# Performance work log

Measured on AMD Instinct MI355X. Metric: run time of the kernel, lower is better.

## Reference

```python
import jax, jax.numpy as jnp
import numpy as np

D_MODEL = 512
NUM_HEADS = 8
D_HEAD = 64
BATCH = 2
SEQ = 2048
NEG_BIG = 1.0e10


def setup_inputs() -> dict:
    key = jax.random.key(0)
    k1, k2, k3, k4, k5 = jax.random.split(key, 5)
    scale = D_MODEL ** -0.5
    return {
        "x": jax.random.normal(k1, (BATCH, SEQ, D_MODEL), dtype=jnp.float32),
        "W_Q": jax.random.normal(k2, (NUM_HEADS, D_HEAD, D_MODEL), dtype=jnp.float32) * scale,
        "W_K": jax.random.normal(k3, (NUM_HEADS, D_HEAD, D_MODEL), dtype=jnp.float32) * scale,
        "W_V": jax.random.normal(k4, (NUM_HEADS, D_HEAD, D_MODEL), dtype=jnp.float32) * scale,
        "W_O": jax.random.normal(k5, (D_MODEL, D_HEAD * NUM_HEADS), dtype=jnp.float32) * scale,
    }


def reference(x, W_Q, W_K, W_V, W_O):
    b, n, d = x.shape
    # q,k,v: [b, heads, pos, d_head]
    q = jnp.einsum('ihd,bpd->biph', W_Q, x)
    k = jnp.einsum('ihd,bpd->biph', W_K, x)
    v = jnp.einsum('ihd,bpd->biph', W_V, x)
    # scores: [b, heads, q_pos, k_pos]
    scores = jnp.einsum('biph,biqh->biqp', k, q)
    tril = jnp.tril(jnp.ones((n, n), dtype=scores.dtype))   # keep p <= q
    triu = jnp.triu(jnp.ones((n, n), dtype=scores.dtype))   # buffer 'mask'
    # Faithful to source: tril(scores) - 1e10 * (1 - triu)
    masked = scores * tril - NEG_BIG * (1.0 - triu)
    attn = jax.nn.softmax(masked / (D_HEAD ** 0.5), axis=-1)
    z = jnp.einsum('biph,biqp->biqh', v, attn)               # [b, i, q, h]
    z_flat = jnp.transpose(z, (0, 2, 1, 3)).reshape(b, n, -1)  # [b, q, i*h]
    out = jnp.einsum('df,bqf->bqd', W_O, z_flat)
    return out
```

## Files before the change

kernel.cpp:

```cpp
#include <hip/hip_runtime.h>
#include <stdint.h>

#define BATCH 2
#define SEQ 2048
#define DM 512
#define NH 8
#define DH 64
#define MROWS (BATCH * SEQ)
#define NCHUNK 64
#define CHUNK (SEQ / NCHUNK)

typedef __attribute__((ext_vector_type(8))) short bf16x8;
typedef __attribute__((ext_vector_type(4))) float f32x4;

__device__ __forceinline__ unsigned short f2bf(float f) {
    union { float f; uint32_t u; } x; x.f = f;
    uint32_t r = x.u + 0x7fffu + ((x.u >> 16) & 1u);
    return (unsigned short)(r >> 16);
}
__device__ __forceinline__ float bf2f(unsigned short s) {
    union { uint32_t u; float f; } x; x.u = ((uint32_t)s) << 16;
    return x.f;
}

__device__ __forceinline__ void gl_lds16(const void* g, void* l) {
    __builtin_amdgcn_global_load_lds(
        (const __attribute__((address_space(1))) void*)(uintptr_t)g,
        (__attribute__((address_space(3))) void*)(uint32_t)(uintptr_t)l,
        16, 0, 0);
}

__global__ void cvt_all(const float4* __restrict__ x,
                        const float4* __restrict__ Wq, const float4* __restrict__ Wk,
                        const float4* __restrict__ Wv, const float4* __restrict__ Wo,
                        ushort4* __restrict__ xb, ushort4* __restrict__ wb) {
    int i = blockIdx.x * blockDim.x + threadIdx.x;
    float4 v; ushort4* dst; int off;
    if (i < 524288) {
        v = x[i]; dst = xb; off = i;
    } else {
        int j = i - 524288;
        if (j < 131072) {
            int head = j >> 14, rp = (j >> 7) & 127, colq = j & 127;
            v = (rp < 64) ? Wq[head * 8192 + rp * 128 + colq]
                          : Wk[head * 8192 + (rp - 64) * 128 + colq];
        } else if (j < 196608) {
            v = Wv[j - 131072];
        } else {
            v = Wo[j - 196608];
        }
        dst = wb; off = j;
    }
    ushort4 o; o.x = f2bf(v.x); o.y = f2bf(v.y); o.z = f2bf(v.z); o.w = f2bf(v.w);
    dst[off] = o;
}

__global__ __launch_bounds__(256) void proj(
    const unsigned short* __restrict__ xb, const unsigned short* __restrict__ wb,
    float* __restrict__ cA, float* __restrict__ cW,
    unsigned short* __restrict__ V, float* __restrict__ csum)
{
    __shared__ __align__(16) unsigned short S[256 * 32];
    const int t = threadIdx.x, lane = t & 63, wave = t >> 6;
    const int lr = lane >> 2, lc = (lane & 3) * 8;
    const int bid = blockIdx.x;
    const int wm = wave * 32;
    const int kcol = (lane >> 4) * 8;
    const int l15 = lane & 15;

    if (bid < 256) {
        const int head = bid & 7, m0 = (bid >> 3) * 128;
        const unsigned short* B = wb + head * 65536;
        const unsigned short* gb[4];
#pragma unroll
        for (int r = 0; r < 4; r++) {
            int grow = r * 64 + wave * 16 + lr;
            gb[r] = (grow < 128) ? xb + (size_t)(m0 + grow) * 512 + lc
                                 : B + (size_t)(grow - 128) * 512 + lc;
        }
        f32x4 acc[2][8];
#pragma unroll
        for (int i = 0; i < 2; i++)
#pragma unroll
            for (int j = 0; j < 8; j++) { f32x4 z = {0.f,0.f,0.f,0.f}; acc[i][j] = z; }
        for (int k0 = 0; k0 < 512; k0 += 32) {
            __syncthreads();
#pragma unroll
            for (int r = 0; r < 4; r++)
                gl_lds16(gb[r] + k0, S + (r * 64 + wave * 16) * 32);
            __syncthreads();
            bf16x8 af[2], bfr[8];
#pragma unroll
            for (int i = 0; i < 2; i++)
                af[i] = *(const bf16x8*)(S + (wm + i * 16 + l15) * 32 + kcol);
#pragma unroll
            for (int j = 0; j < 8; j++)
                bfr[j] = *(const bf16x8*)(S + (128 + j * 16 + l15) * 32 + kcol);
#pragma unroll
            for (int i = 0; i < 2; i++)
#pragma unroll
                for (int j = 0; j < 8; j++)
                    acc[i][j] = __builtin_amdgcn_mfma_f32_16x16x32_bf16(af[i], bfr[j], acc[i][j], 0, 0, 0);
        }
#pragma unroll
        for (int i = 0; i < 2; i++)
#pragma unroll
            for (int r = 0; r < 4; r++) {
                float d = 0.f;
#pragma unroll
                for (int j = 0; j < 4; j++) d += acc[i][j][r] * acc[i][j + 4][r];
                d += __shfl_xor(d, 1); d += __shfl_xor(d, 2);
                d += __shfl_xor(d, 4); d += __shfl_xor(d, 8);
                if (l15 == 0) {
                    int row = m0 + wm + i * 16 + (lane >> 4) * 4 + r;
                    int p = row & (SEQ - 1);
                    float dd = d * 0.125f;
                    float M = fmaxf(dd, 0.f);
                    float a = expf(dd - M), e0 = expf(-M);
                    float Z = a + (float)(SEQ - 1 - p) * e0;
                    cA[row * NH + head] = a / Z;
                    cW[row * NH + head] = e0 / Z;
                }
            }
    } else {
        const int b2 = bid - 256;
        const int head = b2 & 7, m0 = (b2 >> 3) * 128, n0 = head * 64;
        const unsigned short* B = wb + 524288 + (size_t)n0 * 512;
        const unsigned short* gb[3];
#pragma unroll
        for (int r = 0; r < 3; r++) {
            int grow = r * 64 + wave * 16 + lr;
            gb[r] = (grow < 128) ? xb + (size_t)(m0 + grow) * 512 + lc
                                 : B + (size_t)(grow - 128) * 512 + lc;
        }
        f32x4 acc[2][4];
#pragma unroll
        for (int i = 0; i < 2; i++)
#pragma unroll
            for (int j = 0; j < 4; j++) { f32x4 z = {0.f,0.f,0.f,0.f}; acc[i][j] = z; }
        for (int k0 = 0; k0 < 512; k0 += 32) {
            __syncthreads();
#pragma unroll
            for (int r = 0; r < 3; r++)
                gl_lds16(gb[r] + k0, S + (r * 64 + wave * 16) * 32);
            __syncthreads();
            bf16x8 af[2], bfr[4];
#pragma unroll
            for (int i = 0; i < 2; i++)
                af[i] = *(const bf16x8*)(S + (wm + i * 16 + l15) * 32 + kcol);
#pragma unroll
            for (int j = 0; j < 4; j++)
                bfr[j] = *(const bf16x8*)(S + (128 + j * 16 + l15) * 32 + kcol);
#pragma unroll
            for (int i = 0; i < 2; i++)
#pragma unroll
                for (int j = 0; j < 4; j++)
                    acc[i][j] = __builtin_amdgcn_mfma_f32_16x16x32_bf16(af[i], bfr[j], acc[i][j], 0, 0, 0);
        }
        const int crow = m0 + wm + (lane >> 4) * 4;
#pragma unroll
        for (int i = 0; i < 2; i++)
#pragma unroll
            for (int j = 0; j < 4; j++)
#pragma unroll
                for (int r = 0; r < 4; r++)
                    V[(size_t)(crow + i * 16 + r) * DM + n0 + j * 16 + l15] = f2bf(acc[i][j][r]);
        float s[4];
#pragma unroll
        for (int j = 0; j < 4; j++) {
            s[j] = 0.f;
#pragma unroll
            for (int i = 0; i < 2; i++)
#pragma unroll
                for (int r = 0; r < 4; r++) s[j] += acc[i][j][r];
            s[j] += __shfl_xor(s[j], 16);
            s[j] += __shfl_xor(s[j], 32);
        }
        if (lane < 16) {
            int bi = (m0 >> 11) * NH + head;
            int chunk = ((m0 & (SEQ - 1)) >> 5) + wave;
#pragma unroll
            for (int j = 0; j < 4; j++)
                csum[(bi * NCHUNK + chunk) * 64 + j * 16 + lane] = s[j];
        }
    }
}

__global__ __launch_bounds__(256) void zbuild(
    const unsigned short* __restrict__ V, const float* __restrict__ csum,
    const float* __restrict__ cA, const float* __restrict__ cW,
    unsigned short* __restrict__ Zb) {
    int ci = blockIdx.x * 4 + (threadIdx.x >> 6);
    int h = threadIdx.x & 63;
    int c = ci & (NCHUNK - 1), bi = ci >> 6;
    int i = bi & 7, b = bi >> 3;
    float r = 0.f;
    for (int cc = c + 1; cc < NCHUNK; cc++) r += csum[((bi << 6) + cc) * 64 + h];
    for (int j = CHUNK - 1; j >= 0; j--) {
        int p = c * CHUNK + j;
        size_t row = (size_t)(b * SEQ + p);
        float v = bf2f(V[row * DM + i * DH + h]);
        float a = cA[row * NH + i], w = cW[row * NH + i];
        Zb[row * DM + i * DH + h] = f2bf(fmaf(a, v, w * r));
        r += v;
    }
}

template<int TM, int TN, int WM, int WN>
__global__ __launch_bounds__(256) void gemm_bt(
    const unsigned short* __restrict__ A, const unsigned short* __restrict__ B,
    float* __restrict__ C, int M, int N, int K)
{
    constexpr int ROWS = TM + TN;
    constexpr int ROUNDS = ROWS / 64;
    constexpr int MI = WM / 16, NJ = WN / 16;
    constexpr int WAVES_N = TN / WN;
    __shared__ __align__(16) unsigned short S[ROWS * 32];
    const int t = threadIdx.x, lane = t & 63, wave = t >> 6;
    const int wm = (wave / WAVES_N) * WM, wn = (wave % WAVES_N) * WN;
    const int m0 = blockIdx.x * TM, n0 = blockIdx.y * TN;
    const int lr = lane >> 2, lc = (lane & 3) * 8;

    const unsigned short* gbase[ROUNDS];
#pragma unroll
    for (int r = 0; r < ROUNDS; r++) {
        int grow = r * 64 + wave * 16 + lr;
        gbase[r] = (grow < TM) ? A + (size_t)(m0 + grow) * K + lc
                               : B + (size_t)(n0 + grow - TM) * K + lc;
    }

    f32x4 acc[MI][NJ];
#pragma unroll
    for (int i = 0; i < MI; i++)
#pragma unroll
        for (int j = 0; j < NJ; j++) { f32x4 z = {0.f,0.f,0.f,0.f}; acc[i][j] = z; }

    const int mrow = wm + (lane & 15);
    const int nrow = TM + wn + (lane & 15);
    const int kcol = (lane >> 4) * 8;

    for (int k0 = 0; k0 < K; k0 += 32) {
        __syncthreads();
#pragma unroll
        for (int r = 0; r < ROUNDS; r++)
            gl_lds16(gbase[r] + k0, S + (r * 64 + wave * 16) * 32);
        __syncthreads();
        bf16x8 af[MI], bfr[NJ];
#pragma unroll
        for (int i = 0; i < MI; i++)
            af[i] = *(const bf16x8*)(S + (mrow + i * 16) * 32 + kcol);
#pragma unroll
        for (int j = 0; j < NJ; j++)
            bfr[j] = *(const bf16x8*)(S + (nrow + j * 16) * 32 + kcol);
#pragma unroll
        for (int i = 0; i < MI; i++)
#pragma unroll
            for (int j = 0; j < NJ; j++)
                acc[i][j] = __builtin_amdgcn_mfma_f32_16x16x32_bf16(af[i], bfr[j], acc[i][j], 0, 0, 0);
    }
    const int crow = m0 + wm + (lane >> 4) * 4;
    const int ccol = n0 + wn + (lane & 15);
#pragma unroll
    for (int i = 0; i < MI; i++)
#pragma unroll
        for (int j = 0; j < NJ; j++)
#pragma unroll
            for (int r = 0; r < 4; r++)
                C[(size_t)(crow + i * 16 + r) * N + ccol + j * 16] = acc[i][j][r];
}

extern "C" void kernel_launch(void* const* d_in, const int* in_sizes, int n_in,
                              void* d_out, int out_size, void* d_ws, size_t ws_size,
                              hipStream_t stream) {
    const float* x  = (const float*)d_in[0];
    const float* Wq = (const float*)d_in[1];
    const float* Wk = (const float*)d_in[2];
    const float* Wv = (const float*)d_in[3];
    const float* Wo = (const float*)d_in[4];
    float* out = (float*)d_out;
    char* ws = (char*)d_ws;

    unsigned short* xb = (unsigned short*)(ws);
    unsigned short* wb = (unsigned short*)(ws + 4194304);
    unsigned short* V  = (unsigned short*)(ws + 6291456);
    float* cA = (float*)(ws + 10485760);
    float* cW = (float*)(ws + 10616832);
    float* cs = (float*)(ws + 10747904);
    unsigned short* Zb = (unsigned short*)(ws + 11010048);

    cvt_all<<<3072, 256, 0, stream>>>((const float4*)x, (const float4*)Wq,
                                      (const float4*)Wk, (const float4*)Wv,
                                      (const float4*)Wo, (ushort4*)xb, (ushort4*)wb);
    proj<<<512, 256, 0, stream>>>(xb, wb, cA, cW, V, cs);
    zbuild<<<256, 256, 0, stream>>>(V, cs, cA, cW, Zb);
    gemm_bt<64, 64, 32, 32><<<dim3(64, 8, 1), 256, 0, stream>>>(
        Zb, wb + 786432, out, MROWS, DM, DM);
}
```

Baseline: 114.7 us.

## Fuse Q/K/V projections into one uniform block type, double scan chunks

The weight conversion now interleaves Wq, Wk and Wv per head. Each proj block therefore computes Q, K and V for a 64-row tile in a single pass, replacing the earlier split into separate QK and V block types. This removes the duplicate staging of the x tile across the two block types and gives every block the same amount of work. The chunk count for the suffix-sum scan doubles to 128, so zbuild runs twice as many blocks, each with a shorter serial loop, at the cost of a longer per-chunk csum reduction.

```diff
diff --git a/kernel.cpp b/kernel.cpp
--- a/kernel.cpp
+++ b/kernel.cpp
@@ -7,7 +7,7 @@
 #define NH 8
 #define DH 64
 #define MROWS (BATCH * SEQ)
-#define NCHUNK 64
+#define NCHUNK 128
 #define CHUNK (SEQ / NCHUNK)
 
 typedef __attribute__((ext_vector_type(8))) short bf16x8;
@@ -40,12 +40,13 @@
         v = x[i]; dst = xb; off = i;
     } else {
         int j = i - 524288;
-        if (j < 131072) {
-            int head = j >> 14, rp = (j >> 7) & 127, colq = j & 127;
-            v = (rp < 64) ? Wq[head * 8192 + rp * 128 + colq]
-                          : Wk[head * 8192 + (rp - 64) * 128 + colq];
-        } else if (j < 196608) {
-            v = Wv[j - 131072];
+        if (j < 196608) {
+            int head = j / 24576;
+            int rem = j - head * 24576;
+            int rp = rem >> 7, colq = rem & 127;
+            const float4* src = (rp < 64) ? Wq : (rp < 128) ? Wk : Wv;
+            int r2 = (rp < 64) ? rp : (rp < 128) ? rp - 64 : rp - 128;
+            v = src[head * 8192 + r2 * 128 + colq];
         } else {
             v = Wo[j - 196608];
         }
@@ -63,126 +64,74 @@
     __shared__ __align__(16) unsigned short S[256 * 32];
     const int t = threadIdx.x, lane = t & 63, wave = t >> 6;
     const int lr = lane >> 2, lc = (lane & 3) * 8;
-    const int bid = blockIdx.x;
-    const int wm = wave * 32;
-    const int kcol = (lane >> 4) * 8;
-    const int l15 = lane & 15;
-
-    if (bid < 256) {
-        const int head = bid & 7, m0 = (bid >> 3) * 128;
-        const unsigned short* B = wb + head * 65536;
-        const unsigned short* gb[4];
-#pragma unroll
-        for (int r = 0; r < 4; r++) {
-            int grow = r * 64 + wave * 16 + lr;
-            gb[r] = (grow < 128) ? xb + (size_t)(m0 + grow) * 512 + lc
-                                 : B + (size_t)(grow - 128) * 512 + lc;
+    const int head = blockIdx.x & 7, m0 = (blockIdx.x >> 3) * 64;
+    const int wm = wave * 16, l15 = lane & 15, kcol = (lane >> 4) * 8;
+    const unsigned short* B = wb + head * 98304;
+
+    const unsigned short* gb[4];
+#pragma unroll
+    for (int r = 0; r < 4; r++) {
+        int grow = r * 64 + wave * 16 + lr;
+        gb[r] = (grow < 64) ? xb + (size_t)(m0 + grow) * 512 + lc
+                            : B + (size_t)(grow - 64) * 512 + lc;
+    }
+
+    f32x4 acc[12];
+#pragma unroll
+    for (int j = 0; j < 12; j++) { f32x4 z = {0.f, 0.f, 0.f, 0.f}; acc[j] = z; }
+
+    for (int k0 = 0; k0 < 512; k0 += 32) {
+        __syncthreads();
+#pragma unroll
+        for (int r = 0; r < 4; r++)
+            gl_lds16(gb[r] + k0, S + (r * 64 + wave * 16) * 32);
+        __syncthreads();
+        bf16x8 af = *(const bf16x8*)(S + (wm + l15) * 32 + kcol);
+        bf16x8 bfr[12];
+#pragma unroll
+        for (int j = 0; j < 12; j++)
+            bfr[j] = *(const bf16x8*)(S + (64 + j * 16 + l15) * 32 + kcol);
+#pragma unroll
+        for (int j = 0; j < 12; j++)
+            acc[j] = __builtin_amdgcn_mfma_f32_16x16x32_bf16(af, bfr[j], acc[j], 0, 0, 0);
+    }
+    const int crow = m0 + wm + (lane >> 4) * 4;
+#pragma unroll
+    for (int r = 0; r < 4; r++) {
+        float d = 0.f;
+#pragma unroll
+        for (int j = 0; j < 4; j++) d += acc[j][r] * acc[j + 4][r];
+        d += __shfl_xor(d, 1); d += __shfl_xor(d, 2);
+        d += __shfl_xor(d, 4); d += __shfl_xor(d, 8);
+        if (l15 == 0) {
+            int row = crow + r;
+            int p = row & (SEQ - 1);
+            float dd = d * 0.125f;
+            float M = fmaxf(dd, 0.f);
+            float a = expf(dd - M), e0 = expf(-M);
+            float Z = a + (float)(SEQ - 1 - p) * e0;
+            cA[row * NH + head] = a / Z;
+            cW[row * NH + head] = e0 / Z;
         }
-        f32x4 acc[2][8];
-#pragma unroll
-        for (int i = 0; i < 2; i++)
-#pragma unroll
-            for (int j = 0; j < 8; j++) { f32x4 z = {0.f,0.f,0.f,0.f}; acc[i][j] = z; }
-        for (int k0 = 0; k0 < 512; k0 += 32) {
-            __syncthreads();
-#pragma unroll
-            for (int r = 0; r < 4; r++)
-                gl_lds16(gb[r] + k0, S + (r * 64 + wave * 16) * 32);
-            __syncthreads();
-            bf16x8 af[2], bfr[8];
-#pragma unroll
-            for (int i = 0; i < 2; i++)
-                af[i] = *(const bf16x8*)(S + (wm + i * 16 + l15) * 32 + kcol);
-#pragma unroll
-            for (int j = 0; j < 8; j++)
-                bfr[j] = *(const bf16x8*)(S + (128 + j * 16 + l15) * 32 + kcol);
-#pragma unroll
-            for (int i = 0; i < 2; i++)
-#pragma unroll
-                for (int j = 0; j < 8; j++)
-                    acc[i][j] = __builtin_amdgcn_mfma_f32_16x16x32_bf16(af[i], bfr[j], acc[i][j], 0, 0, 0);
-        }
-#pragma unroll
-        for (int i = 0; i < 2; i++)
-#pragma unroll
-            for (int r = 0; r < 4; r++) {
-                float d = 0.f;
-#pragma unroll
-                for (int j = 0; j < 4; j++) d += acc[i][j][r] * acc[i][j + 4][r];
-                d += __shfl_xor(d, 1); d += __shfl_xor(d, 2);
-                d += __shfl_xor(d, 4); d += __shfl_xor(d, 8);
-                if (l15 == 0) {
-                    int row = m0 + wm + i * 16 + (lane >> 4) * 4 + r;
-                    int p = row & (SEQ - 1);
-                    float dd = d * 0.125f;
-                    float M = fmaxf(dd, 0.f);
-                    float a = expf(dd - M), e0 = expf(-M);
-                    float Z = a + (float)(SEQ - 1 - p) * e0;
-                    cA[row * NH + head] = a / Z;
-                    cW[row * NH + head] = e0 / Z;
-                }
-            }
-    } else {
-        const int b2 = bid - 256;
-        const int head = b2 & 7, m0 = (b2 >> 3) * 128, n0 = head * 64;
-        const unsigned short* B = wb + 524288 + (size_t)n0 * 512;
-        const unsigned short* gb[3];
-#pragma unroll
-        for (int r = 0; r < 3; r++) {
-            int grow = r * 64 + wave * 16 + lr;
-            gb[r] = (grow < 128) ? xb + (size_t)(m0 + grow) * 512 + lc
-                                 : B + (size_t)(grow - 128) * 512 + lc;
-        }
-        f32x4 acc[2][4];
-#pragma unroll
-        for (int i = 0; i < 2; i++)
-#pragma unroll
-            for (int j = 0; j < 4; j++) { f32x4 z = {0.f,0.f,0.f,0.f}; acc[i][j] = z; }
-        for (int k0 = 0; k0 < 512; k0 += 32) {
-            __syncthreads();
-#pragma unroll
-            for (int r = 0; r < 3; r++)
-                gl_lds16(gb[r] + k0, S + (r * 64 + wave * 16) * 32);
-            __syncthreads();
-            bf16x8 af[2], bfr[4];
-#pragma unroll
-            for (int i = 0; i < 2; i++)
-                af[i] = *(const bf16x8*)(S + (wm + i * 16 + l15) * 32 + kcol);
-#pragma unroll
-            for (int j = 0; j < 4; j++)
-                bfr[j] = *(const bf16x8*)(S + (128 + j * 16 + l15) * 32 + kcol);
-#pragma unroll
-            for (int i = 0; i < 2; i++)
-#pragma unroll
-                for (int j = 0; j < 4; j++)
-                    acc[i][j] = __builtin_amdgcn_mfma_f32_16x16x32_bf16(af[i], bfr[j], acc[i][j], 0, 0, 0);
-        }
-        const int crow = m0 + wm + (lane >> 4) * 4;
-#pragma unroll
-        for (int i = 0; i < 2; i++)
-#pragma unroll
-            for (int j = 0; j < 4; j++)
-#pragma unroll
-                for (int r = 0; r < 4; r++)
-                    V[(size_t)(crow + i * 16 + r) * DM + n0 + j * 16 + l15] = f2bf(acc[i][j][r]);
-        float s[4];
-#pragma unroll
-        for (int j = 0; j < 4; j++) {
-            s[j] = 0.f;
-#pragma unroll
-            for (int i = 0; i < 2; i++)
-#pragma unroll
-                for (int r = 0; r < 4; r++) s[j] += acc[i][j][r];
-            s[j] += __shfl_xor(s[j], 16);
-            s[j] += __shfl_xor(s[j], 32);
-        }
-        if (lane < 16) {
-            int bi = (m0 >> 11) * NH + head;
-            int chunk = ((m0 & (SEQ - 1)) >> 5) + wave;
-#pragma unroll
-            for (int j = 0; j < 4; j++)
-                csum[(bi * NCHUNK + chunk) * 64 + j * 16 + lane] = s[j];
-        }
+    }
+#pragma unroll
+    for (int j = 0; j < 4; j++)
+#pragma unroll
+        for (int r = 0; r < 4; r++)
+            V[(size_t)(crow + r) * DM + head * DH + j * 16 + l15] = f2bf(acc[8 + j][r]);
+    float s[4];
+#pragma unroll
+    for (int j = 0; j < 4; j++) {
+        s[j] = acc[8 + j][0] + acc[8 + j][1] + acc[8 + j][2] + acc[8 + j][3];
+        s[j] += __shfl_xor(s[j], 16);
+        s[j] += __shfl_xor(s[j], 32);
+    }
+    if (lane < 16) {
+        int bi = (m0 >> 11) * NH + head;
+        int chunk = ((m0 & (SEQ - 1)) >> 4) + wave;
+#pragma unroll
+        for (int j = 0; j < 4; j++)
+            csum[(bi * NCHUNK + chunk) * 64 + j * 16 + lane] = s[j];
     }
 }
 
@@ -192,10 +141,10 @@
     unsigned short* __restrict__ Zb) {
     int ci = blockIdx.x * 4 + (threadIdx.x >> 6);
     int h = threadIdx.x & 63;
-    int c = ci & (NCHUNK - 1), bi = ci >> 6;
+    int c = ci & (NCHUNK - 1), bi = ci >> 7;
     int i = bi & 7, b = bi >> 3;
     float r = 0.f;
-    for (int cc = c + 1; cc < NCHUNK; cc++) r += csum[((bi << 6) + cc) * 64 + h];
+    for (int cc = c + 1; cc < NCHUNK; cc++) r += csum[((bi << 7) + cc) * 64 + h];
     for (int j = CHUNK - 1; j >= 0; j--) {
         int p = c * CHUNK + j;
         size_t row = (size_t)(b * SEQ + p);
@@ -286,13 +235,13 @@
     float* cA = (float*)(ws + 10485760);
     float* cW = (float*)(ws + 10616832);
     float* cs = (float*)(ws + 10747904);
-    unsigned short* Zb = (unsigned short*)(ws + 11010048);
+    unsigned short* Zb = (unsigned short*)(ws + 11272192);
 
     cvt_all<<<3072, 256, 0, stream>>>((const float4*)x, (const float4*)Wq,
                                       (const float4*)Wk, (const float4*)Wv,
                                       (const float4*)Wo, (ushort4*)xb, (ushort4*)wb);
     proj<<<512, 256, 0, stream>>>(xb, wb, cA, cW, V, cs);
-    zbuild<<<256, 256, 0, stream>>>(V, cs, cA, cW, Zb);
+    zbuild<<<512, 256, 0, stream>>>(V, cs, cA, cW, Zb);
     gemm_bt<64, 64, 32, 32><<<dim3(64, 8, 1), 256, 0, stream>>>(
         Zb, wb + 786432, out, MROWS, DM, DM);
 }
```

New measurement: 118.6 us. 3.5% more time.
